# Performance work log

Hardware: AMD Instinct MI355X
Metric: run time of the kernel (lower is better)

The kernel has to match this reference:

```python
import jax, jax.numpy as jnp
import numpy as np

EPS = 1e-5

def setup_inputs() -> dict:
    key = jax.random.key(0)
    k1, k2, k3 = jax.random.split(key, 3)
    B, D, T = 16, 512, 1024
    K = 8192
    x = jax.random.normal(k1, (B, D, T), dtype=jnp.float32)
    embedding_sum = jax.random.normal(k2, (K, D), dtype=jnp.float32)
    cluster_usage = jax.random.uniform(k3, (K,), dtype=jnp.float32)
    return {"x": x, "embedding_sum": embedding_sum, "cluster_usage": cluster_usage}

def reference(x, embedding_sum, cluster_usage):
    # embedding = embedding_sum / clamp(cluster_usage, eps)  -> [K, D]
    emb = embedding_sum / jnp.clip(cluster_usage, EPS, None)[:, None]
    B, D, T = x.shape
    # encode: [B, D, T] -> [B*T, D]
    xf = jnp.transpose(x, (0, 2, 1)).reshape(B * T, D)
    # squared Euclidean distance (argmin-equivalent to cdist p=2)
    x2 = jnp.sum(xf * xf, axis=1, keepdims=True)          # [N, 1]
    e2 = jnp.sum(emb * emb, axis=1)                        # [K]
    d2 = x2 - 2.0 * (xf @ emb.T) + e2[None, :]             # [N, K]
    codes = jnp.argmin(d2, axis=-1).reshape(B, 1, T)       # [B, 1, T]
    # decode: gather codebook vectors
    quantized = emb[codes[:, 0, :]]                        # [B, T, D]
    quantized = jnp.transpose(quantized, (0, 2, 1))        # [B, D, T]
    return codes, quantized
```

## Files before the change

### kernel.cpp

```cpp
#include <hip/hip_runtime.h>
#include <hip/hip_bf16.h>
#include <cfloat>
#include <stdint.h>

#define EPS 1e-5f
constexpr int Dd = 512, Tt = 1024, Kk = 8192;
constexpr int Nq = 16 * 1024;
constexpr float TAU = 1.5f;

typedef __bf16 bf16x8 __attribute__((ext_vector_type(8)));
typedef float  f32x4  __attribute__((ext_vector_type(4)));
typedef unsigned long long u64;

union Pack8 { __bf16 h[8]; int4 v; };

__device__ __forceinline__ void gld16(const void* g, void* l) {
    __builtin_amdgcn_global_load_lds(
        (const __attribute__((address_space(1))) uint32_t*)g,
        (__attribute__((address_space(3))) uint32_t*)l, 16, 0, 0);
}

__device__ __forceinline__ unsigned monokey(float s) {
    unsigned b = __float_as_uint(s);
    return b ^ ((unsigned)((int)b >> 31) | 0x80000000u);
}
__device__ __forceinline__ float unmono(unsigned u) {
    u = (u & 0x80000000u) ? (u ^ 0x80000000u) : ~u;
    return __uint_as_float(u);
}

__device__ __forceinline__ void merge2u(unsigned& a1, unsigned& a2, unsigned b1, unsigned b2) {
    unsigned c1 = min(a1, b1);
    unsigned c2 = min(max(a1, b1), min(a2, b2));
    a1 = c1; a2 = c2;
}
__device__ __forceinline__ u64 umin64(u64 a, u64 b) { return a < b ? a : b; }
__device__ __forceinline__ u64 umax64(u64 a, u64 b) { return a > b ? a : b; }
__device__ __forceinline__ void merge4q(u64& a1, u64& a2, u64& a3, u64& a4,
                                        u64 b1, u64 b2, u64 b3, u64 b4) {
    u64 c1 = umin64(a1, b1);
    u64 c2 = umin64(umin64(a2, b2), umax64(a1, b1));
    u64 c3 = umin64(umin64(a3, b3), umin64(umax64(a2, b1), umax64(a1, b2)));
    u64 c4 = umin64(umin64(a4, b4), umin64(umax64(a3, b1), umax64(a1, b3)));
    c4 = umin64(c4, umax64(a2, b2));
    a1 = c1; a2 = c2; a3 = c3; a4 = c4;
}
__device__ __forceinline__ u64 shflx64(u64 v, int m) {
    int lo = __shfl_xor((int)(unsigned)v, m, 64);
    int hi = __shfl_xor((int)(v >> 32), m, 64);
    return ((u64)(unsigned)hi << 32) | (unsigned)lo;
}

__global__ __launch_bounds__(256) void split_x_kernel(const float* __restrict__ x,
                                                      ushort* __restrict__ Xh,
                                                      float* __restrict__ Xf,
                                                      int* __restrict__ cnt) {
    if (blockIdx.x == 0 && threadIdx.x < 2) cnt[threadIdx.x] = 0;
    __shared__ float Ls[64][68];
    const int tid = threadIdx.x, bid = blockIdx.x;
    const int b  = bid >> 7;
    const int d0 = ((bid >> 4) & 7) * 64;
    const int t0 = (bid & 15) * 64;
    const float* xb = x + ((size_t)b * Dd + d0) * Tt + t0;
#pragma unroll
    for (int it = 0; it < 4; ++it) {
        int s = it * 256 + tid;
        int d = s >> 4, c = (s & 15) * 4;
        float4 g = *(const float4*)(xb + (size_t)d * Tt + c);
        *(float4*)&Ls[d][c] = g;
    }
    __syncthreads();
    const int t = tid >> 2;
    const int dseg = (tid & 3) * 16;
    Pack8 ph[2];
    float vf[16];
#pragma unroll
    for (int dd = 0; dd < 16; ++dd) {
        float v = Ls[dseg + dd][t];
        vf[dd] = v;
        ph[dd >> 3].h[dd & 7] = (__bf16)v;
    }
    size_t base = ((size_t)(b * Tt + t0 + t)) * Dd + d0 + dseg;
    *(int4*)(Xh + base)     = ph[0].v;
    *(int4*)(Xh + base + 8) = ph[1].v;
#pragma unroll
    for (int g = 0; g < 4; ++g)
        *(float4*)(Xf + base + g * 4) = make_float4(vf[g*4], vf[g*4+1], vf[g*4+2], vf[g*4+3]);
}

__global__ __launch_bounds__(256) void split_e_kernel(const float* __restrict__ es,
                                                      const float* __restrict__ usage,
                                                      ushort* __restrict__ Eh,
                                                      float* __restrict__ embf,
                                                      double* __restrict__ e2d,
                                                      float* __restrict__ e2f) {
    const int wave = threadIdx.x >> 6, lane = threadIdx.x & 63;
    const int k = blockIdx.x * 4 + wave;
    const float uc = fmaxf(usage[k], EPS);
    const float* row = es + (size_t)k * Dd;
    const int d = lane * 8;
    float4 a = *(const float4*)(row + d);
    float4 c = *(const float4*)(row + d + 4);
    float ef[8] = {a.x/uc, a.y/uc, a.z/uc, a.w/uc, c.x/uc, c.y/uc, c.z/uc, c.w/uc};
    Pack8 ph;
    double e2 = 0.0;
#pragma unroll
    for (int j = 0; j < 8; ++j) {
        ph.h[j] = (__bf16)ef[j];
        e2 = fma((double)ef[j], (double)ef[j], e2);
    }
    size_t base = (size_t)k * Dd + d;
    *(int4*)(Eh + base) = ph.v;
    *(float4*)(embf + base)     = make_float4(ef[0], ef[1], ef[2], ef[3]);
    *(float4*)(embf + base + 4) = make_float4(ef[4], ef[5], ef[6], ef[7]);
#pragma unroll
    for (int off = 32; off >= 1; off >>= 1) e2 += __shfl_down(e2, off, 64);
    if (lane == 0) { e2d[k] = e2; e2f[k] = (float)e2; }
}

__device__ __forceinline__ void stage_tile(const ushort* __restrict__ Xh,
                                           const ushort* __restrict__ Eh,
                                           char* ldsA, int m0, int n0, int d0, int tid) {
#pragma unroll
    for (int j = 0; j < 4; ++j) {
        int s = j * 512 + tid;
        int row = s >> 3;
        int clog = (s & 7) ^ (row & 7);
        gld16(Xh + (size_t)(m0 + row) * Dd + d0 + clog * 8, ldsA + s * 16);
    }
#pragma unroll
    for (int j = 0; j < 4; ++j) {
        int s = j * 512 + tid;
        int row = s >> 3;
        int clog = (s & 7) ^ (row & 7);
        gld16(Eh + (size_t)(n0 + row) * Dd + d0 + clog * 8, ldsA + 32768 + s * 16);
    }
}

#define SB() __builtin_amdgcn_sched_barrier(0)

__global__ __launch_bounds__(512) void gemm_kernel(const ushort* __restrict__ Xh,
                                                   const ushort* __restrict__ Eh,
                                                   const float* __restrict__ e2f,
                                                   uint2* __restrict__ colres) {
    __shared__ int4 ldsbuf[8192];
    char* lds = (char*)ldsbuf;

    const int tid = threadIdx.x;
    int wg = blockIdx.x;
    int wgid = (wg & 7) * 256 + (wg >> 3);
    int st = wgid >> 5, u = wgid & 31;
    int mb = (st >> 3) * 8 + (u & 7);
    int nb = (st & 7) * 4 + (u >> 3);
    const int m0 = mb * 256, n0 = nb * 256;

    const int wave = tid >> 6, lane = tid & 63;
    const int wm = wave >> 1, wn = wave & 1;
    const int mw = wm * 64, nw = wn * 128;
    const int fm = lane & 15, fq = lane >> 4;
    const int fm7 = fm & 7;
    const int x0 = (fq ^ fm7) * 16;
    const int x1 = ((4 + fq) ^ fm7) * 16;

    f32x4 acc[8][4] = {};

    stage_tile(Xh, Eh, lds,         m0, n0, 0,  tid);
    stage_tile(Xh, Eh, lds + 65536, m0, n0, 64, tid);

    const char* pA0 = lds + (mw + fm) * 128;
    const char* pB0 = lds + 32768 + (nw + fm) * 128;

    for (int t = 0; t < 8; ++t) {
        if (t < 7) asm volatile("s_waitcnt vmcnt(8)" ::: "memory");
        else       asm volatile("s_waitcnt vmcnt(0)" ::: "memory");
        __builtin_amdgcn_s_barrier();
        SB();

        const char* pA = pA0 + (t & 1) * 65536;
        const char* pB = pB0 + (t & 1) * 65536;
        bf16x8 a0[4], a1[4], bl0[4], bh0[4], bl1[4], bh1[4];

#pragma unroll
        for (int i = 0; i < 4; ++i) a0[i]  = *(const bf16x8*)(pA + i * 2048 + x0);
#pragma unroll
        for (int i = 0; i < 4; ++i) bl0[i] = *(const bf16x8*)(pB + i * 2048 + x0);
        SB();
#pragma unroll
        for (int i = 0; i < 4; ++i) bh0[i] = *(const bf16x8*)(pB + 8192 + i * 2048 + x0);
        SB();
#pragma unroll
        for (int i = 0; i < 4; ++i) a1[i]  = *(const bf16x8*)(pA + i * 2048 + x1);
#pragma unroll
        for (int i = 0; i < 4; ++i) bl1[i] = *(const bf16x8*)(pB + i * 2048 + x1);
        SB();

        asm volatile("s_waitcnt lgkmcnt(12)" ::: "memory");
        SB();
        __builtin_amdgcn_s_setprio(1);
#pragma unroll
        for (int i = 0; i < 4; ++i)
#pragma unroll
            for (int j = 0; j < 4; ++j)
                acc[i][j] = __builtin_amdgcn_mfma_f32_16x16x32_bf16(bl0[i], a0[j], acc[i][j], 0, 0, 0);
        __builtin_amdgcn_s_setprio(0);
        SB();

        asm volatile("s_waitcnt lgkmcnt(8)" ::: "memory");
        SB();
        __builtin_amdgcn_s_setprio(1);
#pragma unroll
        for (int i = 0; i < 4; ++i)
#pragma unroll
            for (int j = 0; j < 4; ++j)
                acc[i + 4][j] = __builtin_amdgcn_mfma_f32_16x16x32_bf16(bh0[i], a0[j], acc[i + 4][j], 0, 0, 0);
        __builtin_amdgcn_s_setprio(0);
#pragma unroll
        for (int i = 0; i < 4; ++i) bh1[i] = *(const bf16x8*)(pB + 8192 + i * 2048 + x1);
        SB();

        asm volatile("s_waitcnt lgkmcnt(4)" ::: "memory");
        SB();
        __builtin_amdgcn_s_setprio(1);
#pragma unroll
        for (int i = 0; i < 4; ++i)
#pragma unroll
            for (int j = 0; j < 4; ++j)
                acc[i][j] = __builtin_amdgcn_mfma_f32_16x16x32_bf16(bl1[i], a1[j], acc[i][j], 0, 0, 0);
        __builtin_amdgcn_s_setprio(0);
        SB();

        asm volatile("s_waitcnt lgkmcnt(0)" ::: "memory");
        SB();
        __builtin_amdgcn_s_setprio(1);
#pragma unroll
        for (int i = 0; i < 4; ++i)
#pragma unroll
            for (int j = 0; j < 4; ++j)
                acc[i + 4][j] = __builtin_amdgcn_mfma_f32_16x16x32_bf16(bh1[i], a1[j], acc[i + 4][j], 0, 0, 0);
        __builtin_amdgcn_s_setprio(0);
        SB();
        __builtin_amdgcn_s_barrier();
        if (t + 2 < 8)
            stage_tile(Xh, Eh, lds + (t & 1) * 65536, m0, n0, (t + 2) * 64, tid);
    }

    float4 e2v[8];
#pragma unroll
    for (int ni = 0; ni < 8; ++ni)
        e2v[ni] = *(const float4*)(e2f + n0 + nw + ni * 16 + fq * 4);

    const int cb = (n0 + nw) >> 7;
#pragma unroll
    for (int mj = 0; mj < 4; ++mj) {
        unsigned s1 = 0xFFFFFFFFu, s2 = 0xFFFFFFFFu;
#pragma unroll
        for (int ni = 0; ni < 8; ++ni) {
            unsigned k0 = (monokey(fmaf(-2.0f, acc[ni][mj][0], e2v[ni].x)) & 0xFFFFFF80u) | (unsigned)(ni * 16 + fq * 4 + 0);
            unsigned k1 = (monokey(fmaf(-2.0f, acc[ni][mj][1], e2v[ni].y)) & 0xFFFFFF80u) | (unsigned)(ni * 16 + fq * 4 + 1);
            unsigned k2 = (monokey(fmaf(-2.0f, acc[ni][mj][2], e2v[ni].z)) & 0xFFFFFF80u) | (unsigned)(ni * 16 + fq * 4 + 2);
            unsigned k3 = (monokey(fmaf(-2.0f, acc[ni][mj][3], e2v[ni].w)) & 0xFFFFFF80u) | (unsigned)(ni * 16 + fq * 4 + 3);
            unsigned lo01 = min(k0, k1), hi01 = max(k0, k1);
            unsigned lo23 = min(k2, k3), hi23 = max(k2, k3);
            unsigned p1 = min(lo01, lo23);
            unsigned p2 = min(max(lo01, lo23), min(hi01, hi23));
            merge2u(s1, s2, p1, p2);
        }
#pragma unroll
        for (int stg = 16; stg <= 32; stg <<= 1) {
            unsigned b1 = __shfl_xor(s1, stg, 64);
            unsigned b2 = __shfl_xor(s2, stg, 64);
            merge2u(s1, s2, b1, b2);
        }
        if (lane < 16)
            colres[(size_t)(m0 + mw + mj * 16 + lane) * 64 + cb] = make_uint2(s1, s2);
    }
}

__global__ __launch_bounds__(256) void merge_kernel(const uint2* __restrict__ colres,
                                                    float* __restrict__ out,
                                                    int* __restrict__ cnt,
                                                    int* __restrict__ queueC,
                                                    int* __restrict__ queueF) {
    const int wave = threadIdx.x >> 6, lane = threadIdx.x & 63;
    const int row = blockIdx.x * 4 + wave;
    uint2 q = colres[(size_t)row * 64 + lane];
    const unsigned nb128 = (unsigned)(lane * 128);
    u64 a1 = ((u64)(q.x & 0xFFFFFF80u) << 32) | (nb128 + (q.x & 127u));
    u64 a2 = ((u64)(q.y & 0xFFFFFF80u) << 32) | (nb128 + (q.y & 127u));
    u64 a3 = ~0ull, a4 = ~0ull;
#pragma unroll
    for (int st = 1; st < 64; st <<= 1)
        merge4q(a1, a2, a3, a4, shflx64(a1, st), shflx64(a2, st), shflx64(a3, st), shflx64(a4, st));
    float v1 = unmono((unsigned)(a1 >> 32));
    u64 coll = __ballot(unmono(q.y) < v1 + TAU);
    if (lane == 0) {
        float v2 = unmono((unsigned)(a2 >> 32));
        float v4 = unmono((unsigned)(a4 >> 32));
        int i1 = (int)(unsigned)a1;
        out[row] = (float)i1;
        if (coll != 0ull || (v4 - v1 < TAU)) {
            int p = atomicAdd(&cnt[1], 1);
            queueF[p] = row;
        } else if (v2 - v1 < TAU) {
            int p = atomicAdd(&cnt[0], 1);
            queueC[p * 5]     = row;
            queueC[p * 5 + 1] = i1;
            queueC[p * 5 + 2] = (int)(unsigned)a2;
            queueC[p * 5 + 3] = (int)(unsigned)a3;
            queueC[p * 5 + 4] = (int)(unsigned)a4;
        }
    }
}

__global__ __launch_bounds__(256) void cand_kernel(const float* __restrict__ Xf,
                                                   const float* __restrict__ embf,
                                                   const double* __restrict__ e2d,
                                                   const int* __restrict__ cnt,
                                                   const int* __restrict__ queueC,
                                                   float* __restrict__ out) {
    const int wv = (blockIdx.x << 2) | (threadIdx.x >> 6);
    const int lane = threadIdx.x & 63;
    const int n = cnt[0];
    for (int p = wv; p < n; p += gridDim.x * 4) {
        int row = queueC[p * 5];
        int ci[4] = {queueC[p*5+1], queueC[p*5+2], queueC[p*5+3], queueC[p*5+4]};
        const float* xr = Xf + (size_t)row * Dd + lane * 8;
        float4 xa = *(const float4*)xr;
        float4 xb = *(const float4*)(xr + 4);
        double s[4] = {0.0, 0.0, 0.0, 0.0};
#pragma unroll
        for (int c = 0; c < 4; ++c) {
            const float* er = embf + (size_t)ci[c] * Dd + lane * 8;
            float4 ea = *(const float4*)er;
            float4 eb = *(const float4*)(er + 4);
            double t = 0.0;
            t = fma((double)xa.x, (double)ea.x, t);
            t = fma((double)xa.y, (double)ea.y, t);
            t = fma((double)xa.z, (double)ea.z, t);
            t = fma((double)xa.w, (double)ea.w, t);
            t = fma((double)xb.x, (double)eb.x, t);
            t = fma((double)xb.y, (double)eb.y, t);
            t = fma((double)xb.z, (double)eb.z, t);
            t = fma((double)xb.w, (double)eb.w, t);
            s[c] = t;
        }
#pragma unroll
        for (int off = 32; off >= 1; off >>= 1) {
#pragma unroll
            for (int c = 0; c < 4; ++c) s[c] += __shfl_down(s[c], off, 64);
        }
        if (lane == 0) {
            double bv = DBL_MAX; int bi = 0x7fffffff;
#pragma unroll
            for (int c = 0; c < 4; ++c) {
                double dv = fma(-2.0, s[c], e2d[ci[c]]);
                if (dv < bv || (dv == bv && ci[c] < bi)) { bv = dv; bi = ci[c]; }
            }
            out[row] = (float)bi;
        }
    }
}

__global__ __launch_bounds__(256) void fscan_kernel(const float* __restrict__ Xf,
                                                    const float* __restrict__ embf,
                                                    const double* __restrict__ e2d,
                                                    const int* __restrict__ cnt,
                                                    const int* __restrict__ queueF,
                                                    double* __restrict__ fbv,
                                                    int* __restrict__ fbi) {
    __shared__ float xs[512];
    __shared__ double sv[256];
    __shared__ int si[256];
    const int tid = threadIdx.x;
    const int ntask = cnt[1] * 16;
    for (int task = blockIdx.x; task < ntask; task += gridDim.x) {
        int qi = task >> 4, ch = task & 15;
        int row = queueF[qi];
        __syncthreads();
        for (int d = tid; d < Dd; d += 256)
            xs[d] = Xf[(size_t)row * Dd + d];
        __syncthreads();
        double bv = DBL_MAX; int bi = 0x7fffffff;
#pragma unroll
        for (int c = 0; c < 2; ++c) {
            int k = ch * 512 + c * 256 + tid;
            const float* er = embf + (size_t)k * Dd;
            double a0 = 0, a1 = 0, a2 = 0, a3 = 0;
            for (int d = 0; d < Dd; d += 4) {
                float4 e = *(const float4*)(er + d);
                float4 xv = *(const float4*)&xs[d];
                a0 = fma((double)e.x, (double)xv.x, a0);
                a1 = fma((double)e.y, (double)xv.y, a1);
                a2 = fma((double)e.z, (double)xv.z, a2);
                a3 = fma((double)e.w, (double)xv.w, a3);
            }
            double s = fma(-2.0, (a0 + a1) + (a2 + a3), e2d[k]);
            if (s < bv || (s == bv && k < bi)) { bv = s; bi = k; }
        }
        sv[tid] = bv; si[tid] = bi;
        __syncthreads();
        for (int off = 128; off > 0; off >>= 1) {
            if (tid < off) {
                if (sv[tid + off] < sv[tid] ||
                    (sv[tid + off] == sv[tid] && si[tid + off] < si[tid])) {
                    sv[tid] = sv[tid + off]; si[tid] = si[tid + off];
                }
            }
            __syncthreads();
        }
        if (tid == 0) { fbv[task] = sv[0]; fbi[task] = si[0]; }
    }
}

__global__ void fmerge_kernel(const int* __restrict__ cnt,
                              const int* __restrict__ queueF,
                              const double* __restrict__ fbv,
                              const int* __restrict__ fbi,
                              float* __restrict__ out) {
    const int nF = cnt[1];
    for (int qi = blockIdx.x * 256 + threadIdx.x; qi < nF; qi += gridDim.x * 256) {
        double bv = DBL_MAX; int bi = 0x7fffffff;
        for (int c = 0; c < 16; ++c) {
            double v = fbv[qi * 16 + c]; int i = fbi[qi * 16 + c];
            if (v < bv || (v == bv && i < bi)) { bv = v; bi = i; }
        }
        out[queueF[qi]] = (float)bi;
    }
}

__global__ __launch_bounds__(256) void gather_kernel(const float* __restrict__ embf,
                                                     float* __restrict__ out) {
    __shared__ int cs[64];
    const int tid = threadIdx.x;
    const int m0 = blockIdx.x * 64;
    const int b = m0 >> 10;
    const int t0 = m0 & (Tt - 1);
    if (tid < 64) cs[tid] = (int)out[m0 + tid];
    __syncthreads();
    const int tq = tid & 63;
    const int dg = tid >> 6;
    const int c = cs[tq];
    const float* row = embf + (size_t)c * Dd;
    float* ob = out + Nq + (size_t)b * Dd * Tt + t0 + tq;
#pragma unroll 4
    for (int d = dg * 128; d < dg * 128 + 128; ++d)
        ob[(size_t)d * Tt] = row[d];
}

extern "C" void kernel_launch(void* const* d_in, const int* in_sizes, int n_in,
                              void* d_out, int out_size, void* d_ws, size_t ws_size,
                              hipStream_t stream) {
    const float* x     = (const float*)d_in[0];
    const float* es    = (const float*)d_in[1];
    const float* usage = (const float*)d_in[2];
    float* out = (float*)d_out;

    char* w = (char*)d_ws;
    ushort* Xh = (ushort*)w;   w += (size_t)Nq * Dd * 2;
    ushort* Eh = (ushort*)w;   w += (size_t)Kk * Dd * 2;
    float*  Xf = (float*)w;    w += (size_t)Nq * Dd * 4;
    float*  embf = (float*)w;  w += (size_t)Kk * Dd * 4;
    double* e2d = (double*)w;  w += (size_t)Kk * 8;
    float*  e2f = (float*)w;   w += (size_t)Kk * 4;
    uint2* colres = (uint2*)w; w += (size_t)Nq * 64 * 8;
    int* cnt = (int*)w;        w += 256;
    int* queueC = (int*)w;     w += (size_t)Nq * 5 * 4;
    int* queueF = (int*)w;     w += (size_t)Nq * 4;
    double* fbv = (double*)Xh;
    int*    fbi = (int*)((char*)Xh + 4 * 1024 * 1024);

    split_x_kernel<<<2048, 256, 0, stream>>>(x, Xh, Xf, cnt);
    split_e_kernel<<<Kk / 4, 256, 0, stream>>>(es, usage, Eh, embf, e2d, e2f);
    gemm_kernel<<<2048, 512, 0, stream>>>(Xh, Eh, e2f, colres);
    merge_kernel<<<Nq / 4, 256, 0, stream>>>(colres, out, cnt, queueC, queueF);
    cand_kernel<<<256, 256, 0, stream>>>(Xf, embf, e2d, cnt, queueC, out);
    fscan_kernel<<<256, 256, 0, stream>>>(Xf, embf, e2d, cnt, queueF, fbv, fbi);
    fmerge_kernel<<<64, 256, 0, stream>>>(cnt, queueF, fbv, fbi, out);
    gather_kernel<<<Nq / 64, 256, 0, stream>>>(embf, out);
}
```

Measured before the change: 377.2 us.

## Interleave global-to-LDS staging with MFMA phases in bf16 GEMM main loop

Restructures the GEMM K-loop so that global-to-LDS loads for the next tile are split into quarter chunks and issued between the four MFMA sub-phases, instead of as one bulk stage at the end of each iteration. LDS fragment reads now use a single reused B register set, which lowers register pressure, and each sub-phase adds workgroup barriers. The aim is to spread memory traffic across the compute and keep the MFMA units busier. In exchange there are many more s_barriers per iteration and tighter lgkmcnt waits that may serialize LDS reads with compute.

```diff
diff --git a/kernel.cpp b/kernel.cpp
--- a/kernel.cpp
+++ b/kernel.cpp
@@ -118,22 +118,24 @@
     if (lane == 0) { e2d[k] = e2; e2f[k] = (float)e2; }
 }
 
-__device__ __forceinline__ void stage_tile(const ushort* __restrict__ Xh,
-                                           const ushort* __restrict__ Eh,
-                                           char* ldsA, int m0, int n0, int d0, int tid) {
-#pragma unroll
-    for (int j = 0; j < 4; ++j) {
-        int s = j * 512 + tid;
+__device__ __forceinline__ void stageA2(const ushort* __restrict__ Xh, char* buf,
+                                        int m0, int d0, int tid, int j0) {
+#pragma unroll
+    for (int j = 0; j < 2; ++j) {
+        int s = (j0 + j) * 512 + tid;
         int row = s >> 3;
         int clog = (s & 7) ^ (row & 7);
-        gld16(Xh + (size_t)(m0 + row) * Dd + d0 + clog * 8, ldsA + s * 16);
-    }
-#pragma unroll
-    for (int j = 0; j < 4; ++j) {
-        int s = j * 512 + tid;
+        gld16(Xh + (size_t)(m0 + row) * Dd + d0 + clog * 8, buf + s * 16);
+    }
+}
+__device__ __forceinline__ void stageB2(const ushort* __restrict__ Eh, char* buf,
+                                        int n0, int d0, int tid, int j0) {
+#pragma unroll
+    for (int j = 0; j < 2; ++j) {
+        int s = (j0 + j) * 512 + tid;
         int row = s >> 3;
         int clog = (s & 7) ^ (row & 7);
-        gld16(Eh + (size_t)(n0 + row) * Dd + d0 + clog * 8, ldsA + 32768 + s * 16);
+        gld16(Eh + (size_t)(n0 + row) * Dd + d0 + clog * 8, buf + 32768 + s * 16);
     }
 }
 
@@ -164,71 +166,87 @@
 
     f32x4 acc[8][4] = {};
 
-    stage_tile(Xh, Eh, lds,         m0, n0, 0,  tid);
-    stage_tile(Xh, Eh, lds + 65536, m0, n0, 64, tid);
-
-    const char* pA0 = lds + (mw + fm) * 128;
-    const char* pB0 = lds + 32768 + (nw + fm) * 128;
+    stageA2(Xh, lds, m0, 0, tid, 0);
+    stageA2(Xh, lds, m0, 0, tid, 2);
+    stageB2(Eh, lds, n0, 0, tid, 0);
+    stageB2(Eh, lds, n0, 0, tid, 2);
+    stageA2(Xh, lds + 65536, m0, 64, tid, 0);
+    asm volatile("s_waitcnt vmcnt(2)" ::: "memory");
+    __builtin_amdgcn_s_barrier();
+    SB();
 
     for (int t = 0; t < 8; ++t) {
-        if (t < 7) asm volatile("s_waitcnt vmcnt(8)" ::: "memory");
-        else       asm volatile("s_waitcnt vmcnt(0)" ::: "memory");
-        __builtin_amdgcn_s_barrier();
-        SB();
-
-        const char* pA = pA0 + (t & 1) * 65536;
-        const char* pB = pB0 + (t & 1) * 65536;
-        bf16x8 a0[4], a1[4], bl0[4], bh0[4], bl1[4], bh1[4];
-
-#pragma unroll
-        for (int i = 0; i < 4; ++i) a0[i]  = *(const bf16x8*)(pA + i * 2048 + x0);
-#pragma unroll
-        for (int i = 0; i < 4; ++i) bl0[i] = *(const bf16x8*)(pB + i * 2048 + x0);
-        SB();
-#pragma unroll
-        for (int i = 0; i < 4; ++i) bh0[i] = *(const bf16x8*)(pB + 8192 + i * 2048 + x0);
-        SB();
-#pragma unroll
-        for (int i = 0; i < 4; ++i) a1[i]  = *(const bf16x8*)(pA + i * 2048 + x1);
-#pragma unroll
-        for (int i = 0; i < 4; ++i) bl1[i] = *(const bf16x8*)(pB + i * 2048 + x1);
-        SB();
-
-        asm volatile("s_waitcnt lgkmcnt(12)" ::: "memory");
+        char* bufc = lds + (t & 1) * 65536;
+        char* bufn = lds + ((t + 1) & 1) * 65536;
+        const char* pA = bufc + (mw + fm) * 128;
+        const char* pB = bufc + 32768 + (nw + fm) * 128;
+        const int d1 = (t + 1) * 64, d2 = (t + 2) * 64;
+        bf16x8 a0[4], a1[4], fr[4];
+
+#pragma unroll
+        for (int i = 0; i < 4; ++i) a0[i] = *(const bf16x8*)(pA + i * 2048 + x0);
+#pragma unroll
+        for (int i = 0; i < 4; ++i) fr[i] = *(const bf16x8*)(pB + i * 2048 + x0);
+        SB();
+        if (t + 1 < 8) stageA2(Xh, bufn, m0, d1, tid, 2);
+        SB();
+        __builtin_amdgcn_s_barrier();
+        asm volatile("s_waitcnt lgkmcnt(0)" ::: "memory");
         SB();
         __builtin_amdgcn_s_setprio(1);
 #pragma unroll
         for (int i = 0; i < 4; ++i)
 #pragma unroll
             for (int j = 0; j < 4; ++j)
-                acc[i][j] = __builtin_amdgcn_mfma_f32_16x16x32_bf16(bl0[i], a0[j], acc[i][j], 0, 0, 0);
+                acc[i][j] = __builtin_amdgcn_mfma_f32_16x16x32_bf16(fr[i], a0[j], acc[i][j], 0, 0, 0);
         __builtin_amdgcn_s_setprio(0);
         SB();
-
-        asm volatile("s_waitcnt lgkmcnt(8)" ::: "memory");
+        __builtin_amdgcn_s_barrier();
+
+#pragma unroll
+        for (int i = 0; i < 4; ++i) fr[i] = *(const bf16x8*)(pB + 8192 + i * 2048 + x0);
+        SB();
+        if (t + 1 < 8) stageB2(Eh, bufn, n0, d1, tid, 0);
+        SB();
+        __builtin_amdgcn_s_barrier();
+        asm volatile("s_waitcnt lgkmcnt(0)" ::: "memory");
         SB();
         __builtin_amdgcn_s_setprio(1);
 #pragma unroll
         for (int i = 0; i < 4; ++i)
 #pragma unroll
             for (int j = 0; j < 4; ++j)
-                acc[i + 4][j] = __builtin_amdgcn_mfma_f32_16x16x32_bf16(bh0[i], a0[j], acc[i + 4][j], 0, 0, 0);
+                acc[i + 4][j] = __builtin_amdgcn_mfma_f32_16x16x32_bf16(fr[i], a0[j], acc[i + 4][j], 0, 0, 0);
         __builtin_amdgcn_s_setprio(0);
-#pragma unroll
-        for (int i = 0; i < 4; ++i) bh1[i] = *(const bf16x8*)(pB + 8192 + i * 2048 + x1);
-        SB();
-
-        asm volatile("s_waitcnt lgkmcnt(4)" ::: "memory");
+        SB();
+        __builtin_amdgcn_s_barrier();
+
+#pragma unroll
+        for (int i = 0; i < 4; ++i) a1[i] = *(const bf16x8*)(pA + i * 2048 + x1);
+#pragma unroll
+        for (int i = 0; i < 4; ++i) fr[i] = *(const bf16x8*)(pB + i * 2048 + x1);
+        SB();
+        if (t + 1 < 8) stageB2(Eh, bufn, n0, d1, tid, 2);
+        SB();
+        __builtin_amdgcn_s_barrier();
+        asm volatile("s_waitcnt lgkmcnt(0)" ::: "memory");
         SB();
         __builtin_amdgcn_s_setprio(1);
 #pragma unroll
         for (int i = 0; i < 4; ++i)
 #pragma unroll
             for (int j = 0; j < 4; ++j)
-                acc[i][j] = __builtin_amdgcn_mfma_f32_16x16x32_bf16(bl1[i], a1[j], acc[i][j], 0, 0, 0);
+                acc[i][j] = __builtin_amdgcn_mfma_f32_16x16x32_bf16(fr[i], a1[j], acc[i][j], 0, 0, 0);
         __builtin_amdgcn_s_setprio(0);
         SB();
-
+        __builtin_amdgcn_s_barrier();
+
+#pragma unroll
+        for (int i = 0; i < 4; ++i) fr[i] = *(const bf16x8*)(pB + 8192 + i * 2048 + x1);
+        SB();
+        if (t + 2 < 8) stageA2(Xh, bufc, m0, d2, tid, 0);
+        SB();
+        __builtin_amdgcn_s_barrier();
         asm volatile("s_waitcnt lgkmcnt(0)" ::: "memory");
         SB();
         __builtin_amdgcn_s_setprio(1);
@@ -236,12 +254,12 @@
         for (int i = 0; i < 4; ++i)
 #pragma unroll
             for (int j = 0; j < 4; ++j)
-                acc[i + 4][j] = __builtin_amdgcn_mfma_f32_16x16x32_bf16(bh1[i], a1[j], acc[i + 4][j], 0, 0, 0);
+                acc[i + 4][j] = __builtin_amdgcn_mfma_f32_16x16x32_bf16(fr[i], a1[j], acc[i + 4][j], 0, 0, 0);
         __builtin_amdgcn_s_setprio(0);
         SB();
-        __builtin_amdgcn_s_barrier();
-        if (t + 2 < 8)
-            stage_tile(Xh, Eh, lds + (t & 1) * 65536, m0, n0, (t + 2) * 64, tid);
+        if (t <= 5)      { asm volatile("s_waitcnt vmcnt(2)" ::: "memory"); SB(); }
+        else if (t == 6) { asm volatile("s_waitcnt vmcnt(0)" ::: "memory"); SB(); }
+        if (t < 7) __builtin_amdgcn_s_barrier();
     }
 
     float4 e2v[8];
```

After: 371.6 us. About the same (-1.5%).
